# Optimization experiments

Measured on AMD Instinct MI355X. Metric: run time of the kernel, lower is better.

## Reference

```python
import jax, jax.numpy as jnp
import numpy as np

H = 768      # hidden_size (MambaConfig default)
DI = 500     # intermediate_size (overridden)
N = 16       # state_size
R = 48       # time_step_rank = ceil(768/16)
K = 4        # conv_kernel
LYR = 5      # num_hidden_layers
EPS = 1e-5   # layer_norm_epsilon
B, L, IN = 8, 1024, 4096


def _rmsnorm(x, w):
    v = jnp.mean(jnp.square(x), axis=-1, keepdims=True)
    return x * jax.lax.rsqrt(v + EPS) * w


def _mixer(x, in_proj, conv_w, conv_b, x_proj, dt_w, dt_b, A_log, Dp, out_w):
    # x: [B, L, H]
    proj = x @ in_proj                       # [B, L, 2*DI]
    u, gate = jnp.split(proj, 2, axis=-1)
    # causal depthwise conv1d (torch Conv1d padding=K-1, sliced to L)
    up = jnp.pad(u, ((0, 0), (K - 1, 0), (0, 0)))
    conv = conv_b
    for k in range(K):
        conv = conv + up[:, k:k + x.shape[1], :] * conv_w[:, k]
    u = jax.nn.silu(conv)                    # [B, L, DI]
    ssm = u @ x_proj                         # [B, L, R + 2N]
    dt, Bm, Cm = ssm[..., :R], ssm[..., R:R + N], ssm[..., R + N:]
    dt = jax.nn.softplus(dt @ dt_w + dt_b)   # [B, L, DI]
    A = -jnp.exp(A_log)                      # [DI, N]
    dA = jnp.exp(dt[..., None] * A)          # [B, L, DI, N]
    dBu = dt[..., None] * Bm[:, :, None, :] * u[..., None]  # [B, L, DI, N]

    def step(h, xs):
        dA_t, dBu_t, C_t = xs
        h = dA_t * h + dBu_t                 # [B, DI, N]
        y = jnp.einsum('bdn,bn->bd', h, C_t)
        return h, y

    h0 = jnp.zeros((u.shape[0], DI, N), dtype=u.dtype)
    _, ys = jax.lax.scan(step, h0, (dA.transpose(1, 0, 2, 3),
                                    dBu.transpose(1, 0, 2, 3),
                                    Cm.transpose(1, 0, 2)))
    y = ys.transpose(1, 0, 2)                # [B, L, DI]
    y = y + u * Dp
    y = y * jax.nn.silu(gate)
    return y @ out_w                         # [B, L, H]


def setup_inputs() -> dict:
    key = jax.random.key(0)
    ks = jax.random.split(key, 12)
    s = 0.02
    inputs = jax.random.normal(ks[0], (B, L, IN), jnp.float32)
    W_down = jax.random.normal(ks[1], (IN, H), jnp.float32) * s
    in_proj = jax.random.normal(ks[2], (LYR, H, 2 * DI), jnp.float32) * s
    conv_w = jax.random.normal(ks[3], (LYR, DI, K), jnp.float32) * 0.1
    conv_b = jnp.zeros((LYR, DI), jnp.float32)
    x_proj = jax.random.normal(ks[4], (LYR, DI, R + 2 * N), jnp.float32) * s
    dt_w = jax.random.normal(ks[5], (LYR, R, DI), jnp.float32) * s
    dt_b = jax.random.normal(ks[6], (LYR, DI), jnp.float32) * 0.1
    A_log = jnp.broadcast_to(jnp.log(jnp.arange(1, N + 1, dtype=jnp.float32)),
                             (LYR, DI, N)).copy()
    D_param = jnp.ones((LYR, DI), jnp.float32)
    out_w = jax.random.normal(ks[7], (LYR, DI, H), jnp.float32) * s
    norm_w = jnp.ones((LYR, H), jnp.float32)
    norm_f_w = jnp.ones((H,), jnp.float32)
    W_cls = jax.random.normal(ks[8], (H, 1), jnp.float32) * s
    return dict(inputs=inputs, W_down=W_down, in_proj=in_proj, conv_w=conv_w,
                conv_b=conv_b, x_proj=x_proj, dt_w=dt_w, dt_b=dt_b,
                A_log=A_log, D_param=D_param, out_w=out_w, norm_w=norm_w,
                norm_f_w=norm_f_w, W_cls=W_cls)


def reference(inputs, W_down, in_proj, conv_w, conv_b, x_proj, dt_w, dt_b,
              A_log, D_param, out_w, norm_w, norm_f_w, W_cls):
    x = inputs @ W_down                      # down projection [B, L, H]
    for i in range(LYR):
        x = x + _mixer(_rmsnorm(x, norm_w[i]), in_proj[i], conv_w[i],
                       conv_b[i], x_proj[i], dt_w[i], dt_b[i], A_log[i],
                       D_param[i], out_w[i])
    x = _rmsnorm(x, norm_f_w)
    out = x[:, -1]                           # last token [B, H]
    logits = out @ W_cls                     # [B, 1]
    return logits
```

## Files before the change

kernel.cpp:

```cpp
#include <hip/hip_runtime.h>
#include <hip/hip_bf16.h>

#define BATCH 8
#define SEQL 1024
#define INDIM 4096
#define HDIM 768
#define DI 500
#define NSTATE 16
#define RRANK 48
#define KCONV 4
#define NLAYER 5
#define BL (BATCH * SEQL)

typedef __attribute__((ext_vector_type(8))) short bf16x8;
typedef __attribute__((ext_vector_type(4))) float f32x4;

__device__ __forceinline__ void gl_lds16(const void* g, void* l) {
  __builtin_amdgcn_global_load_lds(
      (const __attribute__((address_space(1))) void*)g,
      (__attribute__((address_space(3))) void*)l, 16, 0, 0);
}

__device__ __forceinline__ unsigned short f2bf(float v) {
  return __hip_bfloat16_raw(__float2bfloat16(v)).x;
}
__device__ __forceinline__ float bf2f(unsigned short h) {
  unsigned int u = ((unsigned int)h) << 16;
  float f;
  memcpy(&f, &u, 4);
  return f;
}

template <int CTRL>
__device__ __forceinline__ float ror_add(float x) {
  int r = __builtin_amdgcn_update_dpp(0, __float_as_int(x), CTRL, 0xf, 0xf,
                                      true);
  return x + __int_as_float(r);
}

template <int EPI>
__global__ __launch_bounds__(256) void gemm_mfma(
    const short* __restrict__ A, const short* __restrict__ Bt,
    float* __restrict__ C, const float* __restrict__ bias,
    unsigned short* __restrict__ D0, unsigned short* __restrict__ D1,
    int M, int N, int K, int lda, int ldb, int ldc) {
  __shared__ short As[3][128 * 32];
  __shared__ short Bs[3][128 * 32];
  const int tid = threadIdx.x;
  const int w = tid >> 6, lane = tid & 63;

  const int gx = gridDim.x;
  const int nwg = gx * gridDim.y;
  int flat = blockIdx.y * gx + blockIdx.x;
  flat = (flat & 7) * (nwg >> 3) + (flat >> 3);
  const int m0 = (flat / gx) * 128, n0 = (flat % gx) * 128;

  const int wr = w >> 1, wc = w & 1;
  f32x4 acc[4][4] = {};

  const int srow = tid >> 2;
  const int cpos = tid & 3;
  const int sc = (cpos ^ ((srow >> 1) & 3)) * 8;
  const short* ga0 = A + (size_t)(m0 + srow) * lda + sc;
  const short* ga1 = A + (size_t)(m0 + 64 + srow) * lda + sc;
  const short* gb0 = Bt + (size_t)(n0 + srow) * ldb + sc;
  const short* gb1 = Bt + (size_t)(n0 + 64 + srow) * ldb + sc;
  const int lr = lane & 15, kb = lane >> 4;
  const int kbx = (kb ^ ((lr >> 1) & 3)) * 8;

  auto stage = [&](int buf, int k0) {
    gl_lds16(ga0 + k0, &As[buf][w * 512]);
    gl_lds16(ga1 + k0, &As[buf][2048 + w * 512]);
    gl_lds16(gb0 + k0, &Bs[buf][w * 512]);
    gl_lds16(gb1 + k0, &Bs[buf][2048 + w * 512]);
  };
  auto compute = [&](int buf) {
    bf16x8 af[4], bfr[4];
#pragma unroll
    for (int i = 0; i < 4; ++i) {
      af[i] = *(const bf16x8*)&As[buf][(wr * 64 + i * 16 + lr) * 32 + kbx];
      bfr[i] = *(const bf16x8*)&Bs[buf][(wc * 64 + i * 16 + lr) * 32 + kbx];
    }
#pragma unroll
    for (int i = 0; i < 4; ++i)
#pragma unroll
      for (int j = 0; j < 4; ++j)
        acc[i][j] = __builtin_amdgcn_mfma_f32_16x16x32_bf16(af[i], bfr[j],
                                                            acc[i][j], 0, 0, 0);
  };

  const int nk = K >> 5;
  stage(0, 0);
  if (nk > 1) stage(1, 32);
  int cur = 0;
  for (int t = 0; t < nk; ++t) {
    if (t + 1 < nk)
      asm volatile("s_waitcnt vmcnt(4)" ::: "memory");
    else
      asm volatile("s_waitcnt vmcnt(0)" ::: "memory");
    __builtin_amdgcn_s_barrier();
    __builtin_amdgcn_sched_barrier(0);
    compute(cur);
    if (t + 2 < nk) {
      int nb = cur + 2;
      if (nb >= 3) nb -= 3;
      stage(nb, (t + 2) * 32);
    }
    ++cur;
    if (cur == 3) cur = 0;
  }

#pragma unroll
  for (int i = 0; i < 4; ++i) {
    const int row = m0 + wr * 64 + i * 16 + (lane >> 4) * 4;
#pragma unroll
    for (int j = 0; j < 4; ++j) {
      const int col = n0 + wc * 64 + j * 16 + (lane & 15);
      if (EPI == 3) {
        if (col < N) {
          float4 v4;
#pragma unroll
          for (int r = 0; r < 4; ++r) {
            float v = acc[i][j][r] + bias[col];
            ((float*)&v4)[r] = (v > 15.f) ? v : log1pf(expf(v));
          }
          const int bb = row >> 10, tt = row & 1023;
          *(float4*)&C[((size_t)bb * DI + col) * 1024 + tt] = v4;
        }
      } else if (EPI == 4) {
#pragma unroll
        for (int r = 0; r < 4; ++r) {
          unsigned short h = f2bf(acc[i][j][r]);
          size_t rr = (size_t)(row + r);
          if (col < DI)
            D0[rr * 512 + col] = h;
          else
            D1[rr * 512 + (col - DI)] = h;
        }
      } else if (EPI == 5) {
#pragma unroll
        for (int r = 0; r < 4; ++r) {
          float v = acc[i][j][r];
          size_t rr = (size_t)(row + r);
          if (col < 64) D0[rr * 64 + col] = f2bf(col < RRANK ? v : 0.f);
          if (col >= RRANK && col < 64) C[rr * 32 + 2 * (col - RRANK)] = v;
          if (col >= 64 && col < 80) C[rr * 32 + 2 * (col - 64) + 1] = v;
        }
      } else {
        if (col < N) {
#pragma unroll
          for (int r = 0; r < 4; ++r) {
            float v = acc[i][j][r];
            size_t idx = (size_t)(row + r) * ldc + col;
            if (EPI == 1) v += C[idx];
            C[idx] = v;
          }
        }
      }
    }
  }
}

__global__ __launch_bounds__(256) void convert_cast(
    const float* __restrict__ src, __hip_bfloat16* __restrict__ dst, long n) {
  long i = ((long)blockIdx.x * 256 + threadIdx.x) * 4;
  if (i >= n) return;
  float4 v = *(const float4*)(src + i);
  dst[i + 0] = __float2bfloat16(v.x);
  dst[i + 1] = __float2bfloat16(v.y);
  dst[i + 2] = __float2bfloat16(v.z);
  dst[i + 3] = __float2bfloat16(v.w);
}

__global__ __launch_bounds__(256) void convert_wT(
    const float* __restrict__ src, __hip_bfloat16* __restrict__ dst, int K,
    int N, int Kpad, int Npad, long src_lstride, long dst_lstride) {
  int idx = blockIdx.x * 256 + threadIdx.x;
  int per = Kpad * Npad;
  if (idx >= per) return;
  const float* s = src + (long)blockIdx.y * src_lstride;
  __hip_bfloat16* d = dst + (long)blockIdx.y * dst_lstride;
  int n = idx / Kpad, k = idx % Kpad;
  float v = (k < K && n < N) ? s[(long)k * N + n] : 0.f;
  d[idx] = __float2bfloat16(v);
}

__device__ __forceinline__ float block_sum256(float v, float* sm) {
#pragma unroll
  for (int off = 32; off > 0; off >>= 1) v += __shfl_down(v, off, 64);
  int wid = threadIdx.x >> 6;
  if ((threadIdx.x & 63) == 0) sm[wid] = v;
  __syncthreads();
  float t = sm[0] + sm[1] + sm[2] + sm[3];
  __syncthreads();
  return t;
}

__global__ __launch_bounds__(256) void rmsnorm_kernel(
    const float* __restrict__ X, const float* __restrict__ w,
    __hip_bfloat16* __restrict__ XN) {
  __shared__ float sm[4];
  const long row = blockIdx.x;
  const float* x = X + row * HDIM;
  float vals[3];
  float s = 0.f;
#pragma unroll
  for (int j = 0; j < 3; ++j) {
    vals[j] = x[threadIdx.x + j * 256];
    s += vals[j] * vals[j];
  }
  float tot = block_sum256(s, sm);
  float scale = rsqrtf(tot / (float)HDIM + 1e-5f);
#pragma unroll
  for (int j = 0; j < 3; ++j) {
    int c = threadIdx.x + j * 256;
    XN[row * HDIM + c] = __float2bfloat16(vals[j] * scale * w[c]);
  }
}

__global__ __launch_bounds__(256) void conv_fused_kernel(
    const unsigned short* __restrict__ Uraw, const float* __restrict__ cw,
    const float* __restrict__ cb, unsigned short* __restrict__ Ubf,
    unsigned short* __restrict__ Ut, int layer) {
  __shared__ unsigned short tin[35][33];
  __shared__ unsigned short tout[32][33];
  const int d0 = blockIdx.x * 32, t0 = blockIdx.y * 32, b = blockIdx.z;
  const int tx = threadIdx.x & 31, ty = threadIdx.x >> 5;
#pragma unroll
  for (int r = 0; r < 5; ++r) {
    int tr = ty + r * 8;
    if (tr < 35) {
      int t = t0 + tr - (KCONV - 1);
      tin[tr][tx] =
          (t >= 0) ? Uraw[((size_t)b * 1024 + t) * 512 + d0 + tx] : 0;
    }
  }
  __syncthreads();
  const int d = d0 + tx;
  float w0 = 0.f, w1 = 0.f, w2 = 0.f, w3 = 0.f, bias = 0.f;
  if (d < DI) {
    const float* w = cw + ((size_t)layer * DI + d) * KCONV;
    w0 = w[0]; w1 = w[1]; w2 = w[2]; w3 = w[3];
    bias = cb[layer * DI + d];
  }
#pragma unroll
  for (int r = 0; r < 4; ++r) {
    const int tt = ty + r * 8;
    unsigned short h = 0;
    if (d < DI) {
      float a = bias + w0 * bf2f(tin[tt][tx]) + w1 * bf2f(tin[tt + 1][tx]) +
                w2 * bf2f(tin[tt + 2][tx]) + w3 * bf2f(tin[tt + 3][tx]);
      h = f2bf(a / (1.f + expf(-a)));
    }
    tout[tt][tx] = h;
    Ubf[((size_t)b * 1024 + t0 + tt) * 512 + d] = h;
  }
  __syncthreads();
#pragma unroll
  for (int r = 0; r < 4; ++r) {
    const int dd = ty + r * 8;
    Ut[((size_t)b * 512 + d0 + dd) * 1024 + t0 + tx] = tout[tx][dd];
  }
}

__global__ __launch_bounds__(256) void y_gate_kernel(
    const unsigned short* __restrict__ Yt, const unsigned short* __restrict__ G,
    unsigned short* __restrict__ Ybf) {
  __shared__ unsigned short tile[32][33];
  const int d0 = blockIdx.x * 32, t0 = blockIdx.y * 32, b = blockIdx.z;
  const int tx = threadIdx.x & 31, ty = threadIdx.x >> 5;
#pragma unroll
  for (int r = 0; r < 4; ++r) {
    int d = d0 + ty + r * 8;
    tile[ty + r * 8][tx] =
        (d < DI) ? Yt[((size_t)b * 512 + d) * 1024 + t0 + tx]
                 : (unsigned short)0;
  }
  __syncthreads();
#pragma unroll
  for (int r = 0; r < 4; ++r) {
    size_t row = (size_t)b * 1024 + t0 + ty + r * 8;
    int d = d0 + tx;
    float yv = 0.f;
    if (d < DI) {
      float y = bf2f(tile[tx][ty + r * 8]);
      float g = bf2f(G[row * 512 + d]);
      yv = y * (g / (1.f + expf(-g)));
    }
    Ybf[row * 512 + d] = f2bf(yv);
  }
}

__global__ __launch_bounds__(512) void scan_kernel(
    const float* __restrict__ DTt, const unsigned short* __restrict__ Ut,
    const float* __restrict__ BC, const float* __restrict__ A_log,
    const float* __restrict__ Dparam, unsigned short* __restrict__ Yt,
    int layer) {
  __shared__ float2 sdtu[1056];
  __shared__ float s_ap[32][17];
  __shared__ float s_h0[32][17];
  __shared__ float s_hi[32][17];
  const int orig = blockIdx.x;
  const int blk = (orig & 7) * (BATCH * DI / 8) + (orig >> 3);
  const int b = blk / DI, d = blk % DI;
  const int tid = threadIdx.x;
  const int c = tid >> 4, n = tid & 15;

  const float* dtp = DTt + ((size_t)b * DI + d) * 1024;
  const unsigned short* up = Ut + ((size_t)b * 512 + d) * 1024;
#pragma unroll
  for (int k = 0; k < 2; ++k) {
    int x = tid + k * 512;
    sdtu[x + (x >> 5)] = make_float2(dtp[x], bf2f(up[x]));
  }
  __syncthreads();

  const float An2 =
      -expf(A_log[((size_t)layer * DI + d) * NSTATE + n]) * 1.44269504f;
  const float Dp = Dparam[layer * DI + d];
  const int t0 = c * 32;
  const float2* sb = sdtu + c * 33;
  const float2* bc = (const float2*)(BC + ((size_t)b * 1024 + t0) * 32) + n;

  float hl[32], appre[32];
  {
    float h = 0.f, ap = 1.f;
#pragma unroll
    for (int s = 0; s < 32; ++s) {
      float2 du = sb[s];
      float a = exp2f(du.x * An2);
      h = a * h + du.x * du.y * bc[s * 16].x;
      ap *= a;
      hl[s] = h;
      appre[s] = ap;
    }
    s_ap[c][n] = ap;
    s_h0[c][n] = h;
  }
  __syncthreads();

  if (tid < 16) {
    float hi = 0.f;
    for (int cc = 0; cc < 32; ++cc) {
      s_hi[cc][tid] = hi;
      hi = s_ap[cc][tid] * hi + s_h0[cc][tid];
    }
  }
  __syncthreads();

  const float h0i = s_hi[c][n];
  const float* cp = (const float*)bc;
  unsigned short* yp = Yt + ((size_t)b * 512 + d) * 1024 + t0;
#pragma unroll
  for (int s = 0; s < 32; s += 2) {
    float ht0 = fmaf(appre[s], h0i, hl[s]);
    float ht1 = fmaf(appre[s + 1], h0i, hl[s + 1]);
    float p0 = ht0 * cp[s * 32 + 1];
    float p1 = ht1 * cp[(s + 1) * 32 + 1];
    p0 = ror_add<0x128>(p0);
    p1 = ror_add<0x128>(p1);
    p0 = ror_add<0x124>(p0);
    p1 = ror_add<0x124>(p1);
    p0 = ror_add<0x122>(p0);
    p1 = ror_add<0x122>(p1);
    p0 = ror_add<0x121>(p0);
    p1 = ror_add<0x121>(p1);
    if (n == 0) {
      float y0 = p0 + sb[s].y * Dp;
      float y1 = p1 + sb[s + 1].y * Dp;
      unsigned int pk =
          (unsigned int)f2bf(y0) | ((unsigned int)f2bf(y1) << 16);
      *(unsigned int*)(yp + s) = pk;
    }
  }
}

__global__ __launch_bounds__(256) void final_kernel(
    const float* __restrict__ X, const float* __restrict__ nfw,
    const float* __restrict__ Wcls, float* __restrict__ out) {
  __shared__ float sm[4];
  const int b = blockIdx.x;
  const long row = (long)b * SEQL + (SEQL - 1);
  const float* x = X + row * HDIM;
  float vals[3];
  float s = 0.f;
#pragma unroll
  for (int j = 0; j < 3; ++j) {
    vals[j] = x[threadIdx.x + j * 256];
    s += vals[j] * vals[j];
  }
  float tot = block_sum256(s, sm);
  float scale = rsqrtf(tot / (float)HDIM + 1e-5f);
  float dot = 0.f;
#pragma unroll
  for (int j = 0; j < 3; ++j) {
    int c = threadIdx.x + j * 256;
    dot += vals[j] * scale * nfw[c] * Wcls[c];
  }
  float td = block_sum256(dot, sm);
  if (threadIdx.x == 0) out[b] = td;
}

extern "C" void kernel_launch(void* const* d_in, const int* in_sizes, int n_in,
                              void* d_out, int out_size, void* d_ws,
                              size_t ws_size, hipStream_t stream) {
  const float* inputs  = (const float*)d_in[0];
  const float* W_down  = (const float*)d_in[1];
  const float* in_proj = (const float*)d_in[2];
  const float* conv_w  = (const float*)d_in[3];
  const float* conv_b  = (const float*)d_in[4];
  const float* x_proj  = (const float*)d_in[5];
  const float* dt_w    = (const float*)d_in[6];
  const float* dt_b    = (const float*)d_in[7];
  const float* A_log   = (const float*)d_in[8];
  const float* D_param = (const float*)d_in[9];
  const float* out_w   = (const float*)d_in[10];
  const float* norm_w  = (const float*)d_in[11];
  const float* norm_fw = (const float*)d_in[12];
  const float* W_cls   = (const float*)d_in[13];
  float* out = (float*)d_out;

  char* ws = (char*)d_ws;
  __hip_bfloat16* Abf   = (__hip_bfloat16*)(ws + 0);
  __hip_bfloat16* Wdbf  = (__hip_bfloat16*)(ws + 67108864);
  __hip_bfloat16* XNbf  = (__hip_bfloat16*)(ws + 0);
  unsigned short* Yt    = (unsigned short*)(ws + 0);
  float*          DTt   = (float*)(ws + 12582912);
  unsigned short* Uraw  = (unsigned short*)(ws + 28966912);
  unsigned short* Ybf   = (unsigned short*)(ws + 28966912);
  unsigned short* Gate  = (unsigned short*)(ws + 37355520);
  unsigned short* Ubf   = (unsigned short*)(ws + 45744128);
  unsigned short* Ut    = (unsigned short*)(ws + 54132736);
  float*          BC    = (float*)(ws + 62521344);
  __hip_bfloat16* SSMbf = (__hip_bfloat16*)(ws + 66715648);
  float*          X     = (float*)(ws + 73400320);
  __hip_bfloat16* inpbf = (__hip_bfloat16*)(ws + 98566144);
  __hip_bfloat16* xpbf  = (__hip_bfloat16*)(ws + 106430464);
  __hip_bfloat16* dtwbf = (__hip_bfloat16*)(ws + 107085824);
  __hip_bfloat16* outwbf= (__hip_bfloat16*)(ws + 107413504);

  convert_cast<<<(long)BL * 4096 / 4 / 256, 256, 0, stream>>>(inputs, Abf,
                                                              (long)BL * 4096);
  convert_wT<<<dim3((768 * 4096 + 255) / 256, 1), 256, 0, stream>>>(
      W_down, Wdbf, 4096, 768, 4096, 768, 0, 0);
  convert_wT<<<dim3((768 * 1024 + 255) / 256, NLAYER), 256, 0, stream>>>(
      in_proj, inpbf, 768, 1000, 768, 1024, (long)HDIM * 1000, 768 * 1024);
  convert_wT<<<dim3((128 * 512 + 255) / 256, NLAYER), 256, 0, stream>>>(
      x_proj, xpbf, 500, 80, 512, 128, (long)DI * 80, 128 * 512);
  convert_wT<<<dim3((512 * 64 + 255) / 256, NLAYER), 256, 0, stream>>>(
      dt_w, dtwbf, 48, 500, 64, 512, (long)RRANK * DI, 512 * 64);
  convert_wT<<<dim3((768 * 512 + 255) / 256, NLAYER), 256, 0, stream>>>(
      out_w, outwbf, 500, 768, 512, 768, (long)DI * HDIM, 768 * 512);

  gemm_mfma<0><<<dim3(768 / 128, BL / 128), 256, 0, stream>>>(
      (const short*)Abf, (const short*)Wdbf, X, nullptr, nullptr, nullptr, BL,
      HDIM, INDIM, INDIM, INDIM, HDIM);

  for (int i = 0; i < NLAYER; ++i) {
    rmsnorm_kernel<<<BL, 256, 0, stream>>>(X, norm_w + i * HDIM, XNbf);
    gemm_mfma<4><<<dim3(1024 / 128, BL / 128), 256, 0, stream>>>(
        (const short*)XNbf, (const short*)(inpbf + (long)i * 768 * 1024),
        nullptr, nullptr, Uraw, Gate, BL, 1000, HDIM, HDIM, HDIM, 0);
    conv_fused_kernel<<<dim3(16, 32, 8), 256, 0, stream>>>(Uraw, conv_w,
                                                           conv_b, Ubf, Ut, i);
    gemm_mfma<5><<<dim3(1, BL / 128), 256, 0, stream>>>(
        (const short*)Ubf, (const short*)(xpbf + (long)i * 128 * 512), BC,
        nullptr, (unsigned short*)SSMbf, nullptr, BL, 80, 512, 512, 512, 0);
    gemm_mfma<3><<<dim3(512 / 128, BL / 128), 256, 0, stream>>>(
        (const short*)SSMbf, (const short*)(dtwbf + (long)i * 512 * 64), DTt,
        dt_b + i * DI, nullptr, nullptr, BL, DI, 64, 64, 64, 0);
    scan_kernel<<<BATCH * DI, 512, 0, stream>>>(DTt, Ut, BC, A_log, D_param,
                                                Yt, i);
    y_gate_kernel<<<dim3(16, 32, 8), 256, 0, stream>>>(Yt, Gate, Ybf);
    gemm_mfma<1><<<dim3(768 / 128, BL / 128), 256, 0, stream>>>(
        (const short*)Ybf, (const short*)(outwbf + (long)i * 768 * 512), X,
        nullptr, nullptr, nullptr, BL, HDIM, 512, 512, 512, HDIM);
  }

  final_kernel<<<BATCH, 256, 0, stream>>>(X, norm_fw, W_cls, out);
}
```

Baseline: 1.146 ms.

## Restructure scan kernel: 4 channels per block, 8 chunks of 128, recompute pass

Each scan block now handles four channels of the inner dimension with 8 time chunks of 128 steps per channel, instead of one channel with 32 chunks of 32. The first pass keeps only the final state and a cumulative dt, and computes the chunk decay as a single exp2 of A times the dt sum. The second pass recomputes the recurrence from the carried-in state rather than storing per-step partial states in registers. This cuts register pressure, the number of blocks, and the length of the serial cross-chunk combine, at the cost of doing the exp and recurrence work twice and running longer serial chains per thread.

Measured after the change: 1.122 ms. 2.1% less time.

```diff
diff --git a/kernel.cpp b/kernel.cpp
--- a/kernel.cpp
+++ b/kernel.cpp
@@ -296,81 +296,89 @@
     const float* __restrict__ BC, const float* __restrict__ A_log,
     const float* __restrict__ Dparam, unsigned short* __restrict__ Yt,
     int layer) {
-  __shared__ float2 sdtu[1056];
-  __shared__ float s_ap[32][17];
-  __shared__ float s_h0[32][17];
-  __shared__ float s_hi[32][17];
+  __shared__ float2 sdtu[4][1036];
+  __shared__ float s_ap[8][4][16];
+  __shared__ float s_h0[8][4][16];
+  __shared__ float s_hi[8][4][16];
   const int orig = blockIdx.x;
-  const int blk = (orig & 7) * (BATCH * DI / 8) + (orig >> 3);
-  const int b = blk / DI, d = blk % DI;
+  const int blk = (orig & 7) * 125 + (orig >> 3);
+  const int b = blk / 125;
+  const int d0 = (blk - b * 125) * 4;
   const int tid = threadIdx.x;
-  const int c = tid >> 4, n = tid & 15;
-
-  const float* dtp = DTt + ((size_t)b * DI + d) * 1024;
-  const unsigned short* up = Ut + ((size_t)b * 512 + d) * 1024;
-#pragma unroll
-  for (int k = 0; k < 2; ++k) {
+  const int c = tid >> 6;
+  const int lane = tid & 63;
+  const int dl = lane >> 4;
+  const int n = lane & 15;
+  const int d = d0 + dl;
+
+#pragma unroll
+  for (int k = 0; k < 8; ++k) {
     int x = tid + k * 512;
-    sdtu[x + (x >> 5)] = make_float2(dtp[x], bf2f(up[x]));
+    int dd = x >> 10, t = x & 1023;
+    float dtv = DTt[((size_t)b * DI + d0 + dd) * 1024 + t];
+    float uv = bf2f(Ut[((size_t)b * 512 + d0 + dd) * 1024 + t]);
+    sdtu[dd][t] = make_float2(dtv, uv);
   }
   __syncthreads();
 
   const float An2 =
       -expf(A_log[((size_t)layer * DI + d) * NSTATE + n]) * 1.44269504f;
   const float Dp = Dparam[layer * DI + d];
-  const int t0 = c * 32;
-  const float2* sb = sdtu + c * 33;
-  const float2* bc = (const float2*)(BC + ((size_t)b * 1024 + t0) * 32) + n;
-
-  float hl[32], appre[32];
+  const int t0 = c * 128;
+  const float2* sb = &sdtu[dl][t0];
+  const float2* bcp = (const float2*)(BC + ((size_t)b * 1024 + t0) * 32) + n;
+
   {
-    float h = 0.f, ap = 1.f;
-#pragma unroll
-    for (int s = 0; s < 32; ++s) {
+    float h = 0.f, cum = 0.f;
+#pragma unroll 8
+    for (int s = 0; s < 128; ++s) {
       float2 du = sb[s];
       float a = exp2f(du.x * An2);
-      h = a * h + du.x * du.y * bc[s * 16].x;
-      ap *= a;
-      hl[s] = h;
-      appre[s] = ap;
-    }
-    s_ap[c][n] = ap;
-    s_h0[c][n] = h;
-  }
-  __syncthreads();
-
-  if (tid < 16) {
+      cum += du.x;
+      h = a * h + du.x * du.y * bcp[s * 16].x;
+    }
+    s_ap[c][dl][n] = exp2f(An2 * cum);
+    s_h0[c][dl][n] = h;
+  }
+  __syncthreads();
+
+  if (tid < 64) {
     float hi = 0.f;
-    for (int cc = 0; cc < 32; ++cc) {
-      s_hi[cc][tid] = hi;
-      hi = s_ap[cc][tid] * hi + s_h0[cc][tid];
-    }
-  }
-  __syncthreads();
-
-  const float h0i = s_hi[c][n];
-  const float* cp = (const float*)bc;
-  unsigned short* yp = Yt + ((size_t)b * 512 + d) * 1024 + t0;
-#pragma unroll
-  for (int s = 0; s < 32; s += 2) {
-    float ht0 = fmaf(appre[s], h0i, hl[s]);
-    float ht1 = fmaf(appre[s + 1], h0i, hl[s + 1]);
-    float p0 = ht0 * cp[s * 32 + 1];
-    float p1 = ht1 * cp[(s + 1) * 32 + 1];
-    p0 = ror_add<0x128>(p0);
-    p1 = ror_add<0x128>(p1);
-    p0 = ror_add<0x124>(p0);
-    p1 = ror_add<0x124>(p1);
-    p0 = ror_add<0x122>(p0);
-    p1 = ror_add<0x122>(p1);
-    p0 = ror_add<0x121>(p0);
-    p1 = ror_add<0x121>(p1);
-    if (n == 0) {
-      float y0 = p0 + sb[s].y * Dp;
-      float y1 = p1 + sb[s + 1].y * Dp;
-      unsigned int pk =
-          (unsigned int)f2bf(y0) | ((unsigned int)f2bf(y1) << 16);
-      *(unsigned int*)(yp + s) = pk;
+    for (int cc = 0; cc < 8; ++cc) {
+      s_hi[cc][dl][n] = hi;
+      hi = s_ap[cc][dl][n] * hi + s_h0[cc][dl][n];
+    }
+  }
+  __syncthreads();
+
+  {
+    float h = s_hi[c][dl][n];
+    unsigned short* yp = Yt + ((size_t)b * 512 + d) * 1024 + t0;
+#pragma unroll 4
+    for (int s = 0; s < 128; s += 2) {
+      float2 du0 = sb[s], du1 = sb[s + 1];
+      float2 v0 = bcp[s * 16], v1 = bcp[(s + 1) * 16];
+      float a0 = exp2f(du0.x * An2);
+      h = a0 * h + du0.x * du0.y * v0.x;
+      float p0 = h * v0.y;
+      float a1 = exp2f(du1.x * An2);
+      h = a1 * h + du1.x * du1.y * v1.x;
+      float p1 = h * v1.y;
+      p0 = ror_add<0x128>(p0);
+      p1 = ror_add<0x128>(p1);
+      p0 = ror_add<0x124>(p0);
+      p1 = ror_add<0x124>(p1);
+      p0 = ror_add<0x122>(p0);
+      p1 = ror_add<0x122>(p1);
+      p0 = ror_add<0x121>(p0);
+      p1 = ror_add<0x121>(p1);
+      if (n == 0) {
+        float y0 = p0 + du0.y * Dp;
+        float y1 = p1 + du1.y * Dp;
+        unsigned int pk =
+            (unsigned int)f2bf(y0) | ((unsigned int)f2bf(y1) << 16);
+        *(unsigned int*)(yp + s) = pk;
+      }
     }
   }
 }
@@ -469,8 +477,7 @@
     gemm_mfma<3><<<dim3(512 / 128, BL / 128), 256, 0, stream>>>(
         (const short*)SSMbf, (const short*)(dtwbf + (long)i * 512 * 64), DTt,
         dt_b + i * DI, nullptr, nullptr, BL, DI, 64, 64, 64, 0);
-    scan_kernel<<<BATCH * DI, 512, 0, stream>>>(DTt, Ut, BC, A_log, D_param,
-                                                Yt, i);
+    scan_kernel<<<1000, 512, 0, stream>>>(DTt, Ut, BC, A_log, D_param, Yt, i);
     y_gate_kernel<<<dim3(16, 32, 8), 256, 0, stream>>>(Yt, Gate, Ybf);
     gemm_mfma<1><<<dim3(768 / 128, BL / 128), 256, 0, stream>>>(
         (const short*)Ybf, (const short*)(outwbf + (long)i * 768 * 512), X,
```
